# Kernel tuning notes

Measured on AMD Instinct MI355X. Metric: run time of the kernel, lower is better.

## Reference

```python
import jax, jax.numpy as jnp
import numpy as np

B, L, C, H = 4, 2048, 512, 8
D = C // H  # head_dim = 64


def _rope_tables(L, D):
    inv_freq = 1.0 / (10000.0 ** (np.arange(0, D, 2, dtype=np.float32) / D))
    t = np.arange(L, dtype=np.float32)
    freqs = np.outer(t, inv_freq)                      # (L, D/2)
    emb = np.concatenate([freqs, freqs], axis=-1)      # (L, D)
    return jnp.asarray(np.cos(emb)), jnp.asarray(np.sin(emb))


def setup_inputs() -> dict:
    key = jax.random.key(0)
    k1, k2, k3 = jax.random.split(key, 3)
    cos, sin = _rope_tables(L, D)
    return {
        "x": jax.random.normal(k1, (B, L, C), dtype=jnp.float32),
        "qkv_w": jax.random.normal(k2, (3 * C, C), dtype=jnp.float32) * 0.02,
        "qkv_b": jnp.zeros((3 * C,), dtype=jnp.float32),
        "proj_w": jax.random.normal(k3, (C, C), dtype=jnp.float32) * 0.02,
        "proj_b": jnp.zeros((C,), dtype=jnp.float32),
        "cos": cos,
        "sin": sin,
    }


def _rotate_half(x):
    x1, x2 = jnp.split(x, 2, axis=-1)
    return jnp.concatenate([-x2, x1], axis=-1)


def _apply_rope(x, cos, sin):
    # x: (B, H, L, D); cos/sin: (L, D)
    return x * cos[None, None] + _rotate_half(x) * sin[None, None]


def reference(x, qkv_w, qkv_b, proj_w, proj_b, cos, sin):
    b, l, c = x.shape
    scale = 1.0 / jnp.sqrt(jnp.float32(D))
    qkv = x @ qkv_w.T + qkv_b                          # (B, L, 3C)
    qkv = qkv.reshape(b, l, 3, H, D).transpose(2, 0, 3, 1, 4)  # (3, B, H, L, D)
    q, k, v = qkv[0], qkv[1], qkv[2]
    q = _apply_rope(q, cos, sin)
    k = _apply_rope(k, cos, sin)
    attn = jax.nn.softmax(scale * jnp.einsum('bhqd,bhkd->bhqk', q, k), axis=-1)
    out = jnp.einsum('bhqk,bhkd->bhqd', attn, v)       # (B, H, L, D)
    out = out.transpose(0, 2, 1, 3).reshape(b, l, c)   # (B, L, C)
    return out @ proj_w.T + proj_b
```

## Files before the change

### kernel.cpp

```cpp
#include <hip/hip_runtime.h>

#define CDIM 512
#define LDIM 2048
#define BDIM 4
#define HDIM 8
#define DDIM 64

typedef __attribute__((ext_vector_type(8))) short bf16x8;
typedef __attribute__((ext_vector_type(4))) float f32x4;
typedef __attribute__((ext_vector_type(2))) float f32x2;
typedef __attribute__((ext_vector_type(8))) unsigned short ushort8;

static __device__ __forceinline__ unsigned short f2bf(float f) {
  unsigned u = __float_as_uint(f);
  return (unsigned short)((u + 0x7FFFu + ((u >> 16) & 1u)) >> 16);
}

__global__ __launch_bounds__(256) void convert_kernel(
    const float* __restrict__ qw, const float* __restrict__ pw,
    unsigned short* __restrict__ wb, unsigned short* __restrict__ pwb) {
  const size_t i = ((size_t)blockIdx.x * 256 + threadIdx.x) * 8;
  const float* src; unsigned short* dst; size_t off;
  if (i < 786432) { src = qw; dst = wb;  off = i; }
  else            { src = pw; dst = pwb; off = i - 786432; }
  const float4 a = *(const float4*)(src + off);
  const float4 b = *(const float4*)(src + off + 4);
  ushort8 h;
  h[0] = f2bf(a.x); h[1] = f2bf(a.y); h[2] = f2bf(a.z); h[3] = f2bf(a.w);
  h[4] = f2bf(b.x); h[5] = f2bf(b.y); h[6] = f2bf(b.z); h[7] = f2bf(b.w);
  *(ushort8*)(dst + off) = h;
}

__global__ __launch_bounds__(256) void qkv_gemm_kernel(
    const float* __restrict__ x, const unsigned short* __restrict__ wb,
    const float* __restrict__ bias, const float* __restrict__ cosT,
    const float* __restrict__ sinT, unsigned short* __restrict__ qb,
    unsigned short* __restrict__ kb, unsigned short* __restrict__ vt) {
  __shared__ char As[16384];
  __shared__ char Bs[16384];
  const int t  = threadIdx.x;
  const int w  = t >> 6, lane = t & 63;
  const int lo = lane & 15, hi = lane >> 4;
  const int wm = w >> 1, wn = w & 1;
  const int m0 = blockIdx.y * 128, n0 = blockIdx.x * 128;

  f32x4 acc[4][4];
  #pragma unroll
  for (int mt = 0; mt < 4; ++mt)
    #pragma unroll
    for (int nt = 0; nt < 4; ++nt) acc[mt][nt] = (f32x4){0.f, 0.f, 0.f, 0.f};

  const int srow   = t >> 3;
  const int sch    = (t & 7) ^ (srow & 7);
  const char* Bg = (const char*)wb;

  for (int kt = 0; kt < CDIM; kt += 64) {
    #pragma unroll
    for (int s = 0; s < 4; ++s) {
      const int r = s * 32 + srow;
      const float4 f0 = *(const float4*)(x + (size_t)(m0 + r) * CDIM + kt + sch * 8);
      const float4 f1 = *(const float4*)(x + (size_t)(m0 + r) * CDIM + kt + sch * 8 + 4);
      unsigned u0, u1, u2, u3;
      asm("v_cvt_pk_bf16_f32 %0, %1, %2" : "=v"(u0) : "v"(f0.x), "v"(f0.y));
      asm("v_cvt_pk_bf16_f32 %0, %1, %2" : "=v"(u1) : "v"(f0.z), "v"(f0.w));
      asm("v_cvt_pk_bf16_f32 %0, %1, %2" : "=v"(u2) : "v"(f1.x), "v"(f1.y));
      asm("v_cvt_pk_bf16_f32 %0, %1, %2" : "=v"(u3) : "v"(f1.z), "v"(f1.w));
      uint4 uu; uu.x = u0; uu.y = u1; uu.z = u2; uu.w = u3;
      *(uint4*)(As + s * 4096 + t * 16) = uu;
      __builtin_amdgcn_global_load_lds(
          (const __attribute__((address_space(1))) unsigned int*)
              (Bg + (size_t)(n0 + r) * 1024 + kt * 2 + sch * 16),
          (__attribute__((address_space(3))) unsigned int*)(Bs + s * 4096 + w * 1024),
          16, 0, 0);
    }
    __syncthreads();
    #pragma unroll
    for (int ks = 0; ks < 2; ++ks) {
      bf16x8 af[4], bfr[4];
      #pragma unroll
      for (int mt = 0; mt < 4; ++mt)
        af[mt] = *(const bf16x8*)(As + (wm * 64 + mt * 16 + lo) * 128
                                  + (((ks * 4 + hi) ^ (lo & 7)) << 4));
      #pragma unroll
      for (int nt = 0; nt < 4; ++nt)
        bfr[nt] = *(const bf16x8*)(Bs + (wn * 64 + nt * 16 + lo) * 128
                                   + (((ks * 4 + hi) ^ (lo & 7)) << 4));
      #pragma unroll
      for (int mt = 0; mt < 4; ++mt)
        #pragma unroll
        for (int nt = 0; nt < 4; ++nt)
          acc[mt][nt] = __builtin_amdgcn_mfma_f32_16x16x32_bf16(
              af[mt], bfr[nt], acc[mt][nt], 0, 0, 0);
    }
    __syncthreads();
  }

  const int nbase = n0 + wn * 64;
  const int typ   = nbase >> 9;
  const int hh    = (nbase >> 6) & 7;
  const int bb    = m0 >> 11;
  const int lbase = (m0 & 2047) + wm * 64;

  float bq[4];
  #pragma unroll
  for (int nt = 0; nt < 4; ++nt) bq[nt] = bias[nbase + nt * 16 + lo];
  #pragma unroll
  for (int mt = 0; mt < 4; ++mt)
    #pragma unroll
    for (int nt = 0; nt < 4; ++nt)
      #pragma unroll
      for (int reg = 0; reg < 4; ++reg) acc[mt][nt][reg] += bq[nt];

  if (typ == 2) {
    unsigned short* vbase = vt + (size_t)(bb * HDIM + hh) * DDIM * LDIM;
    #pragma unroll
    for (int mt = 0; mt < 4; ++mt)
      #pragma unroll
      for (int nt = 0; nt < 4; ++nt) {
        const int d = nt * 16 + lo;
        #pragma unroll
        for (int reg = 0; reg < 4; ++reg) {
          const int l = lbase + mt * 16 + hi * 4 + reg;
          vbase[(size_t)d * LDIM + l] = f2bf(acc[mt][nt][reg]);
        }
      }
  } else {
    unsigned short* dstb = (typ ? kb : qb) + (size_t)(bb * HDIM + hh) * LDIM * DDIM;
    #pragma unroll
    for (int mt = 0; mt < 4; ++mt)
      #pragma unroll
      for (int nt = 0; nt < 4; ++nt) {
        const int d   = nt * 16 + lo;
        const float sgn = (nt & 2) ? 1.f : -1.f;
        #pragma unroll
        for (int reg = 0; reg < 4; ++reg) {
          const int l = lbase + mt * 16 + hi * 4 + reg;
          const float c = cosT[l * 64 + d], s = sinT[l * 64 + d];
          const float v = acc[mt][nt][reg] * c + sgn * acc[mt][nt ^ 2][reg] * s;
          dstb[(size_t)l * DDIM + d] = f2bf(v);
        }
      }
  }
}

#define CLOG2 0.18033688f

__global__ __launch_bounds__(512) void attn_kernel(
    unsigned short* __restrict__ qb, const unsigned short* __restrict__ kb,
    const unsigned short* __restrict__ vt) {
  __shared__ char Ks[2][8192];
  __shared__ char Vs[2][8192];
  __shared__ char Pw[16384];
  const int t    = threadIdx.x;
  const int w    = t >> 6, lane = t & 63;
  const int lo   = lane & 15, hi = lane >> 4;
  const int bh   = blockIdx.y;
  const int q0   = blockIdx.x * 128 + w * 16;

  const char* Kb = (const char*)kb + (size_t)bh * (LDIM * DDIM * 2);
  const char* Vb = (const char*)vt + (size_t)bh * (LDIM * DDIM * 2);
  unsigned short* Qb = qb + (size_t)bh * (LDIM * DDIM);

  bf16x8 qf[2];
  #pragma unroll
  for (int kd = 0; kd < 2; ++kd)
    qf[kd] = *(const bf16x8*)((const char*)(Qb + (size_t)(q0 + lo) * DDIM)
                              + kd * 64 + hi * 16);

  f32x4 o[4];
  #pragma unroll
  for (int r = 0; r < 4; ++r) o[r] = (f32x4){0.f, 0.f, 0.f, 0.f};
  float mrun = 0.f;
  float mc   = 0.f;
  float lpart = 0.f;

  const int rloc = lane >> 3;
  const int sw   = ((lane & 7) ^ rloc) << 4;
  char* Pwb = Pw + w * 2048;

  auto stage = [&](int tile, int buf) {
    const int r = w * 8 + rloc;
    __builtin_amdgcn_global_load_lds(
        (const __attribute__((address_space(1))) unsigned int*)
            (Kb + (size_t)(tile * 64 + r) * 128 + sw),
        (__attribute__((address_space(3))) unsigned int*)(&Ks[buf][w * 1024]),
        16, 0, 0);
    __builtin_amdgcn_global_load_lds(
        (const __attribute__((address_space(1))) unsigned int*)
            (Vb + (size_t)r * (LDIM * 2) + tile * 128 + sw),
        (__attribute__((address_space(3))) unsigned int*)(&Vs[buf][w * 1024]),
        16, 0, 0);
  };

  stage(0, 0);

  for (int kt = 0; kt < 32; ++kt) {
    const int cur = kt & 1;
    const int nk  = kt < 31 ? kt + 1 : 31;
    stage(nk, cur ^ 1);
    asm volatile("s_waitcnt vmcnt(2)");
    __builtin_amdgcn_s_barrier();
    __builtin_amdgcn_sched_barrier(0);

    f32x4 sv[4];
    __builtin_amdgcn_s_setprio(1);
    #pragma unroll
    for (int nt = 0; nt < 4; ++nt) {
      sv[nt] = (f32x4){0.f, 0.f, 0.f, 0.f};
      const int key = nt * 16 + lo;
      #pragma unroll
      for (int kd = 0; kd < 2; ++kd) {
        const bf16x8 kf = *(const bf16x8*)(&Ks[cur][0] + key * 128
                            + (((kd * 4 + hi) ^ (key & 7)) << 4));
        sv[nt] = __builtin_amdgcn_mfma_f32_16x16x32_bf16(kf, qf[kd], sv[nt], 0, 0, 0);
      }
    }
    __builtin_amdgcn_s_setprio(0);

    const float* sflat = (const float*)sv;
    const f32x2 cc2 = {CLOG2, CLOG2};
    const f32x2 mm2 = {-mc, -mc};
    float pv[16];
    float ps = 0.f;
    #pragma unroll
    for (int i = 0; i < 8; ++i) {
      f32x2 a; a[0] = sflat[2*i]; a[1] = sflat[2*i+1];
      f32x2 xr;
      asm("v_pk_fma_f32 %0, %1, %2, %3" : "=v"(xr) : "v"(a), "v"(cc2), "v"(mm2));
      float p0, p1;
      asm("v_exp_f32 %0, %1" : "=v"(p0) : "v"(xr[0]));
      asm("v_exp_f32 %0, %1" : "=v"(p1) : "v"(xr[1]));
      pv[2*i] = p0; pv[2*i+1] = p1;
      ps += p0; ps += p1;
    }

    if (__builtin_expect((bool)__ballot(ps > 65536.f), 0)) {
      float mx = -1e30f;
      #pragma unroll
      for (int i = 0; i < 16; ++i) mx = fmaxf(mx, sflat[i]);
      mx = fmaxf(mx, __shfl_xor(mx, 16));
      mx = fmaxf(mx, __shfl_xor(mx, 32));
      const float newm = fmaxf(mrun, mx);
      const float al   = exp2f((mrun - newm) * CLOG2);
      lpart *= al;
      #pragma unroll
      for (int r = 0; r < 4; ++r) {
        const float aq = __shfl(al, (hi << 2) + r);
        #pragma unroll
        for (int dt = 0; dt < 4; ++dt) o[dt][r] *= aq;
      }
      mrun = newm;
      mc   = mrun * CLOG2;
      ps = 0.f;
      #pragma unroll
      for (int i = 0; i < 16; ++i) {
        const float p = exp2f(fmaf(sflat[i], CLOG2, -mc));
        pv[i] = p;
        ps += p;
      }
    }
    lpart += ps;

    #pragma unroll
    for (int nt = 0; nt < 4; ++nt) {
      unsigned w0, w1;
      asm("v_cvt_pk_bf16_f32 %0, %1, %2"
          : "=v"(w0) : "v"(pv[nt*4+0]), "v"(pv[nt*4+1]));
      asm("v_cvt_pk_bf16_f32 %0, %1, %2"
          : "=v"(w1) : "v"(pv[nt*4+2]), "v"(pv[nt*4+3]));
      uint2 d2; d2.x = w0; d2.y = w1;
      *(uint2*)(Pwb + lo * 128 + ((nt * 32 + hi * 8) ^ ((lo & 7) << 4))) = d2;
    }

    __builtin_amdgcn_s_setprio(1);
    #pragma unroll
    for (int ks = 0; ks < 2; ++ks) {
      const bf16x8 pf = *(const bf16x8*)(Pwb + lo * 128
                          + (((ks * 4 + hi) ^ (lo & 7)) << 4));
      #pragma unroll
      for (int dt = 0; dt < 4; ++dt) {
        const int d = dt * 16 + lo;
        const bf16x8 vf = *(const bf16x8*)(&Vs[cur][0] + d * 128
                            + (((ks * 4 + hi) ^ (d & 7)) << 4));
        o[dt] = __builtin_amdgcn_mfma_f32_16x16x32_bf16(pf, vf, o[dt], 0, 0, 0);
      }
    }
    __builtin_amdgcn_s_setprio(0);

    __builtin_amdgcn_sched_barrier(0);
    __builtin_amdgcn_s_barrier();
  }

  float rsum = lpart;
  rsum += __shfl_xor(rsum, 16);
  rsum += __shfl_xor(rsum, 32);
  #pragma unroll
  for (int r = 0; r < 4; ++r) {
    const float lr  = __shfl(rsum, (hi << 2) + r);
    const float inv = 1.f / lr;
    const int q = q0 + hi * 4 + r;
    #pragma unroll
    for (int dt = 0; dt < 4; ++dt)
      Qb[(size_t)q * DDIM + dt * 16 + lo] = f2bf(o[dt][r] * inv);
  }
}

__global__ __launch_bounds__(256) void proj_gemm_kernel(
    const unsigned short* __restrict__ ab, const unsigned short* __restrict__ pwb,
    const float* __restrict__ bias, float* __restrict__ out) {
  __shared__ char As[16384];
  __shared__ char Bs[16384];
  const int t  = threadIdx.x;
  const int w  = t >> 6, lane = t & 63;
  const int lo = lane & 15, hi = lane >> 4;
  const int wm = w >> 1, wn = w & 1;
  const int m0 = blockIdx.y * 128, n0 = blockIdx.x * 128;

  f32x4 acc[4][4];
  #pragma unroll
  for (int mt = 0; mt < 4; ++mt)
    #pragma unroll
    for (int nt = 0; nt < 4; ++nt) acc[mt][nt] = (f32x4){0.f, 0.f, 0.f, 0.f};

  const int srow   = t >> 3;
  const int schunk = ((t & 7) ^ (srow & 7)) << 4;
  const char* Ag = (const char*)ab;
  const char* Bg = (const char*)pwb;

  for (int kt = 0; kt < CDIM; kt += 64) {
    const int hh = kt >> 6;
    #pragma unroll
    for (int s = 0; s < 4; ++s) {
      const int r = s * 32 + srow;
      const int m = m0 + r;
      const int bb = m >> 11, l = m & 2047;
      __builtin_amdgcn_global_load_lds(
          (const __attribute__((address_space(1))) unsigned int*)
              (Ag + ((size_t)(bb * HDIM + hh) * LDIM + l) * 128 + schunk),
          (__attribute__((address_space(3))) unsigned int*)(As + s * 4096 + w * 1024),
          16, 0, 0);
      __builtin_amdgcn_global_load_lds(
          (const __attribute__((address_space(1))) unsigned int*)
              (Bg + (size_t)(n0 + r) * 1024 + kt * 2 + schunk),
          (__attribute__((address_space(3))) unsigned int*)(Bs + s * 4096 + w * 1024),
          16, 0, 0);
    }
    __syncthreads();
    #pragma unroll
    for (int ks = 0; ks < 2; ++ks) {
      bf16x8 af[4], bfr[4];
      #pragma unroll
      for (int mt = 0; mt < 4; ++mt)
        af[mt] = *(const bf16x8*)(As + (wm * 64 + mt * 16 + lo) * 128
                                  + (((ks * 4 + hi) ^ (lo & 7)) << 4));
      #pragma unroll
      for (int nt = 0; nt < 4; ++nt)
        bfr[nt] = *(const bf16x8*)(Bs + (wn * 64 + nt * 16 + lo) * 128
                                   + (((ks * 4 + hi) ^ (lo & 7)) << 4));
      #pragma unroll
      for (int mt = 0; mt < 4; ++mt)
        #pragma unroll
        for (int nt = 0; nt < 4; ++nt)
          acc[mt][nt] = __builtin_amdgcn_mfma_f32_16x16x32_bf16(
              af[mt], bfr[nt], acc[mt][nt], 0, 0, 0);
    }
    __syncthreads();
  }

  const int nn = n0 + wn * 64;
  float bp[4];
  #pragma unroll
  for (int nt = 0; nt < 4; ++nt) bp[nt] = bias[nn + nt * 16 + lo];
  #pragma unroll
  for (int mt = 0; mt < 4; ++mt)
    #pragma unroll
    for (int nt = 0; nt < 4; ++nt)
      #pragma unroll
      for (int reg = 0; reg < 4; ++reg) {
        const int m = m0 + wm * 64 + mt * 16 + hi * 4 + reg;
        out[(size_t)m * CDIM + nn + nt * 16 + lo] = acc[mt][nt][reg] + bp[nt];
      }
}

extern "C" void kernel_launch(void* const* d_in, const int* in_sizes, int n_in,
                              void* d_out, int out_size, void* d_ws, size_t ws_size,
                              hipStream_t stream) {
  const float* x      = (const float*)d_in[0];
  const float* qkv_w  = (const float*)d_in[1];
  const float* qkv_b  = (const float*)d_in[2];
  const float* proj_w = (const float*)d_in[3];
  const float* proj_b = (const float*)d_in[4];
  const float* cosT   = (const float*)d_in[5];
  const float* sinT   = (const float*)d_in[6];
  float* out = (float*)d_out;

  unsigned short* qb  = (unsigned short*)d_ws;
  unsigned short* kb  = qb + (size_t)BDIM * HDIM * LDIM * DDIM;
  unsigned short* vt  = kb + (size_t)BDIM * HDIM * LDIM * DDIM;
  unsigned short* wb  = vt + (size_t)BDIM * HDIM * LDIM * DDIM;
  unsigned short* pwb = wb + (size_t)3 * CDIM * CDIM;

  convert_kernel<<<dim3(512), 256, 0, stream>>>(qkv_w, proj_w, wb, pwb);
  qkv_gemm_kernel<<<dim3(12, 64), 256, 0, stream>>>(x, wb, qkv_b, cosT, sinT,
                                                    qb, kb, vt);
  attn_kernel<<<dim3(16, 32), 512, 0, stream>>>(qb, kb, vt);
  proj_gemm_kernel<<<dim3(4, 64), 256, 0, stream>>>(qb, pwb, proj_b, out);
}
```

Measured before the change: 110.1 us.

## Give each attention wave two 16-row query groups to reuse K/V fragments

After: 117.3 us. +6.6%, slower.

```diff
diff --git a/kernel.cpp b/kernel.cpp
--- a/kernel.cpp
+++ b/kernel.cpp
@@ -145,7 +145,7 @@
 
 #define CLOG2 0.18033688f
 
-__global__ __launch_bounds__(512) void attn_kernel(
+__global__ __launch_bounds__(256) void attn_kernel(
     unsigned short* __restrict__ qb, const unsigned short* __restrict__ kb,
     const unsigned short* __restrict__ vt) {
   __shared__ char Ks[2][8192];
@@ -155,41 +155,46 @@
   const int w    = t >> 6, lane = t & 63;
   const int lo   = lane & 15, hi = lane >> 4;
   const int bh   = blockIdx.y;
-  const int q0   = blockIdx.x * 128 + w * 16;
+  const int q0   = blockIdx.x * 128 + w * 32;
 
   const char* Kb = (const char*)kb + (size_t)bh * (LDIM * DDIM * 2);
   const char* Vb = (const char*)vt + (size_t)bh * (LDIM * DDIM * 2);
   unsigned short* Qb = qb + (size_t)bh * (LDIM * DDIM);
 
-  bf16x8 qf[2];
-  #pragma unroll
-  for (int kd = 0; kd < 2; ++kd)
-    qf[kd] = *(const bf16x8*)((const char*)(Qb + (size_t)(q0 + lo) * DDIM)
-                              + kd * 64 + hi * 16);
-
-  f32x4 o[4];
-  #pragma unroll
-  for (int r = 0; r < 4; ++r) o[r] = (f32x4){0.f, 0.f, 0.f, 0.f};
-  float mrun = 0.f;
-  float mc   = 0.f;
-  float lpart = 0.f;
+  bf16x8 qf[2][2];
+  #pragma unroll
+  for (int g = 0; g < 2; ++g)
+    #pragma unroll
+    for (int kd = 0; kd < 2; ++kd)
+      qf[g][kd] = *(const bf16x8*)((const char*)(Qb + (size_t)(q0 + g * 16 + lo) * DDIM)
+                                   + kd * 64 + hi * 16);
+
+  f32x4 o[2][4];
+  float mrun[2] = {0.f, 0.f}, mc[2] = {0.f, 0.f}, lpart[2] = {0.f, 0.f};
+  #pragma unroll
+  for (int g = 0; g < 2; ++g)
+    #pragma unroll
+    for (int r = 0; r < 4; ++r) o[g][r] = (f32x4){0.f, 0.f, 0.f, 0.f};
 
   const int rloc = lane >> 3;
   const int sw   = ((lane & 7) ^ rloc) << 4;
-  char* Pwb = Pw + w * 2048;
+  char* Pwb = Pw + w * 4096;
 
   auto stage = [&](int tile, int buf) {
-    const int r = w * 8 + rloc;
-    __builtin_amdgcn_global_load_lds(
-        (const __attribute__((address_space(1))) unsigned int*)
-            (Kb + (size_t)(tile * 64 + r) * 128 + sw),
-        (__attribute__((address_space(3))) unsigned int*)(&Ks[buf][w * 1024]),
-        16, 0, 0);
-    __builtin_amdgcn_global_load_lds(
-        (const __attribute__((address_space(1))) unsigned int*)
-            (Vb + (size_t)r * (LDIM * 2) + tile * 128 + sw),
-        (__attribute__((address_space(3))) unsigned int*)(&Vs[buf][w * 1024]),
-        16, 0, 0);
+    #pragma unroll
+    for (int s = 0; s < 2; ++s) {
+      const int r = w * 16 + s * 8 + rloc;
+      __builtin_amdgcn_global_load_lds(
+          (const __attribute__((address_space(1))) unsigned int*)
+              (Kb + (size_t)(tile * 64 + r) * 128 + sw),
+          (__attribute__((address_space(3))) unsigned int*)(&Ks[buf][(w * 2 + s) * 1024]),
+          16, 0, 0);
+      __builtin_amdgcn_global_load_lds(
+          (const __attribute__((address_space(1))) unsigned int*)
+              (Vb + (size_t)r * (LDIM * 2) + tile * 128 + sw),
+          (__attribute__((address_space(3))) unsigned int*)(&Vs[buf][(w * 2 + s) * 1024]),
+          16, 0, 0);
+    }
   };
 
   stage(0, 0);
@@ -198,91 +203,100 @@
     const int cur = kt & 1;
     const int nk  = kt < 31 ? kt + 1 : 31;
     stage(nk, cur ^ 1);
-    asm volatile("s_waitcnt vmcnt(2)");
+    asm volatile("s_waitcnt vmcnt(4)");
     __builtin_amdgcn_s_barrier();
     __builtin_amdgcn_sched_barrier(0);
 
-    f32x4 sv[4];
+    f32x4 sv[2][4];
     __builtin_amdgcn_s_setprio(1);
     #pragma unroll
     for (int nt = 0; nt < 4; ++nt) {
-      sv[nt] = (f32x4){0.f, 0.f, 0.f, 0.f};
+      sv[0][nt] = (f32x4){0.f, 0.f, 0.f, 0.f};
+      sv[1][nt] = (f32x4){0.f, 0.f, 0.f, 0.f};
       const int key = nt * 16 + lo;
       #pragma unroll
       for (int kd = 0; kd < 2; ++kd) {
         const bf16x8 kf = *(const bf16x8*)(&Ks[cur][0] + key * 128
                             + (((kd * 4 + hi) ^ (key & 7)) << 4));
-        sv[nt] = __builtin_amdgcn_mfma_f32_16x16x32_bf16(kf, qf[kd], sv[nt], 0, 0, 0);
+        sv[0][nt] = __builtin_amdgcn_mfma_f32_16x16x32_bf16(kf, qf[0][kd], sv[0][nt], 0, 0, 0);
+        sv[1][nt] = __builtin_amdgcn_mfma_f32_16x16x32_bf16(kf, qf[1][kd], sv[1][nt], 0, 0, 0);
       }
     }
     __builtin_amdgcn_s_setprio(0);
 
-    const float* sflat = (const float*)sv;
-    const f32x2 cc2 = {CLOG2, CLOG2};
-    const f32x2 mm2 = {-mc, -mc};
-    float pv[16];
-    float ps = 0.f;
-    #pragma unroll
-    for (int i = 0; i < 8; ++i) {
-      f32x2 a; a[0] = sflat[2*i]; a[1] = sflat[2*i+1];
-      f32x2 xr;
-      asm("v_pk_fma_f32 %0, %1, %2, %3" : "=v"(xr) : "v"(a), "v"(cc2), "v"(mm2));
-      float p0, p1;
-      asm("v_exp_f32 %0, %1" : "=v"(p0) : "v"(xr[0]));
-      asm("v_exp_f32 %0, %1" : "=v"(p1) : "v"(xr[1]));
-      pv[2*i] = p0; pv[2*i+1] = p1;
-      ps += p0; ps += p1;
-    }
-
-    if (__builtin_expect((bool)__ballot(ps > 65536.f), 0)) {
-      float mx = -1e30f;
-      #pragma unroll
-      for (int i = 0; i < 16; ++i) mx = fmaxf(mx, sflat[i]);
-      mx = fmaxf(mx, __shfl_xor(mx, 16));
-      mx = fmaxf(mx, __shfl_xor(mx, 32));
-      const float newm = fmaxf(mrun, mx);
-      const float al   = exp2f((mrun - newm) * CLOG2);
-      lpart *= al;
-      #pragma unroll
-      for (int r = 0; r < 4; ++r) {
-        const float aq = __shfl(al, (hi << 2) + r);
-        #pragma unroll
-        for (int dt = 0; dt < 4; ++dt) o[dt][r] *= aq;
-      }
-      mrun = newm;
-      mc   = mrun * CLOG2;
-      ps = 0.f;
-      #pragma unroll
-      for (int i = 0; i < 16; ++i) {
-        const float p = exp2f(fmaf(sflat[i], CLOG2, -mc));
-        pv[i] = p;
-        ps += p;
-      }
-    }
-    lpart += ps;
-
-    #pragma unroll
-    for (int nt = 0; nt < 4; ++nt) {
-      unsigned w0, w1;
-      asm("v_cvt_pk_bf16_f32 %0, %1, %2"
-          : "=v"(w0) : "v"(pv[nt*4+0]), "v"(pv[nt*4+1]));
-      asm("v_cvt_pk_bf16_f32 %0, %1, %2"
-          : "=v"(w1) : "v"(pv[nt*4+2]), "v"(pv[nt*4+3]));
-      uint2 d2; d2.x = w0; d2.y = w1;
-      *(uint2*)(Pwb + lo * 128 + ((nt * 32 + hi * 8) ^ ((lo & 7) << 4))) = d2;
+    #pragma unroll
+    for (int g = 0; g < 2; ++g) {
+      const float* sflat = (const float*)sv[g];
+      const f32x2 cc2 = {CLOG2, CLOG2};
+      const f32x2 mm2 = {-mc[g], -mc[g]};
+      float pv[16];
+      float ps = 0.f;
+      #pragma unroll
+      for (int i = 0; i < 8; ++i) {
+        f32x2 a; a[0] = sflat[2*i]; a[1] = sflat[2*i+1];
+        f32x2 xr;
+        asm("v_pk_fma_f32 %0, %1, %2, %3" : "=v"(xr) : "v"(a), "v"(cc2), "v"(mm2));
+        float p0, p1;
+        asm("v_exp_f32 %0, %1" : "=v"(p0) : "v"(xr[0]));
+        asm("v_exp_f32 %0, %1" : "=v"(p1) : "v"(xr[1]));
+        pv[2*i] = p0; pv[2*i+1] = p1;
+        ps += p0; ps += p1;
+      }
+
+      if (__builtin_expect((bool)__ballot(ps > 65536.f), 0)) {
+        float mx = -1e30f;
+        #pragma unroll
+        for (int i = 0; i < 16; ++i) mx = fmaxf(mx, sflat[i]);
+        mx = fmaxf(mx, __shfl_xor(mx, 16));
+        mx = fmaxf(mx, __shfl_xor(mx, 32));
+        const float newm = fmaxf(mrun[g], mx);
+        const float al   = exp2f((mrun[g] - newm) * CLOG2);
+        lpart[g] *= al;
+        #pragma unroll
+        for (int r = 0; r < 4; ++r) {
+          const float aq = __shfl(al, (hi << 2) + r);
+          #pragma unroll
+          for (int dt = 0; dt < 4; ++dt) o[g][dt][r] *= aq;
+        }
+        mrun[g] = newm;
+        mc[g]   = mrun[g] * CLOG2;
+        ps = 0.f;
+        #pragma unroll
+        for (int i = 0; i < 16; ++i) {
+          const float p = exp2f(fmaf(sflat[i], CLOG2, -mc[g]));
+          pv[i] = p;
+          ps += p;
+        }
+      }
+      lpart[g] += ps;
+
+      #pragma unroll
+      for (int nt = 0; nt < 4; ++nt) {
+        unsigned w0, w1;
+        asm("v_cvt_pk_bf16_f32 %0, %1, %2"
+            : "=v"(w0) : "v"(pv[nt*4+0]), "v"(pv[nt*4+1]));
+        asm("v_cvt_pk_bf16_f32 %0, %1, %2"
+            : "=v"(w1) : "v"(pv[nt*4+2]), "v"(pv[nt*4+3]));
+        uint2 d2; d2.x = w0; d2.y = w1;
+        *(uint2*)(Pwb + g * 2048 + lo * 128
+                  + ((nt * 32 + hi * 8) ^ ((lo & 7) << 4))) = d2;
+      }
     }
 
     __builtin_amdgcn_s_setprio(1);
     #pragma unroll
     for (int ks = 0; ks < 2; ++ks) {
-      const bf16x8 pf = *(const bf16x8*)(Pwb + lo * 128
-                          + (((ks * 4 + hi) ^ (lo & 7)) << 4));
+      const bf16x8 pf0 = *(const bf16x8*)(Pwb + lo * 128
+                           + (((ks * 4 + hi) ^ (lo & 7)) << 4));
+      const bf16x8 pf1 = *(const bf16x8*)(Pwb + 2048 + lo * 128
+                           + (((ks * 4 + hi) ^ (lo & 7)) << 4));
       #pragma unroll
       for (int dt = 0; dt < 4; ++dt) {
         const int d = dt * 16 + lo;
         const bf16x8 vf = *(const bf16x8*)(&Vs[cur][0] + d * 128
                             + (((ks * 4 + hi) ^ (d & 7)) << 4));
-        o[dt] = __builtin_amdgcn_mfma_f32_16x16x32_bf16(pf, vf, o[dt], 0, 0, 0);
+        o[0][dt] = __builtin_amdgcn_mfma_f32_16x16x32_bf16(pf0, vf, o[0][dt], 0, 0, 0);
+        o[1][dt] = __builtin_amdgcn_mfma_f32_16x16x32_bf16(pf1, vf, o[1][dt], 0, 0, 0);
       }
     }
     __builtin_amdgcn_s_setprio(0);
@@ -291,17 +305,20 @@
     __builtin_amdgcn_s_barrier();
   }
 
-  float rsum = lpart;
-  rsum += __shfl_xor(rsum, 16);
-  rsum += __shfl_xor(rsum, 32);
-  #pragma unroll
-  for (int r = 0; r < 4; ++r) {
-    const float lr  = __shfl(rsum, (hi << 2) + r);
-    const float inv = 1.f / lr;
-    const int q = q0 + hi * 4 + r;
-    #pragma unroll
-    for (int dt = 0; dt < 4; ++dt)
-      Qb[(size_t)q * DDIM + dt * 16 + lo] = f2bf(o[dt][r] * inv);
+  #pragma unroll
+  for (int g = 0; g < 2; ++g) {
+    float rsum = lpart[g];
+    rsum += __shfl_xor(rsum, 16);
+    rsum += __shfl_xor(rsum, 32);
+    #pragma unroll
+    for (int r = 0; r < 4; ++r) {
+      const float lr  = __shfl(rsum, (hi << 2) + r);
+      const float inv = 1.f / lr;
+      const int q = q0 + g * 16 + hi * 4 + r;
+      #pragma unroll
+      for (int dt = 0; dt < 4; ++dt)
+        Qb[(size_t)q * DDIM + dt * 16 + lo] = f2bf(o[g][dt][r] * inv);
+    }
   }
 }
 
@@ -403,6 +420,6 @@
   convert_kernel<<<dim3(512), 256, 0, stream>>>(qkv_w, proj_w, wb, pwb);
   qkv_gemm_kernel<<<dim3(12, 64), 256, 0, stream>>>(x, wb, qkv_b, cosT, sinT,
                                                     qb, kb, vt);
-  attn_kernel<<<dim3(16, 32), 512, 0, stream>>>(qb, kb, vt);
+  attn_kernel<<<dim3(16, 32), 256, 0, stream>>>(qb, kb, vt);
   proj_gemm_kernel<<<dim3(4, 64), 256, 0, stream>>>(qb, pwb, proj_b, out);
 }
```
